# Kernel optimization log

Hardware: AMD Instinct MI355X
Metric: run time of the kernel (lower is better)

The kernel has to match this reference:

```python
import jax, jax.numpy as jnp
import numpy as np

_S2 = 2.0 ** -0.5
_S3 = 3.0 ** -0.5
_S6 = 6.0 ** -0.5
# fairchem cg_change_mat(2): (9 decomposed) -> (9 cartesian, row-major 3x3)
_CG = np.array([
    [_S3, 0, 0, 0, _S3, 0, 0, 0, _S3],
    [0, 0, 0, 0, 0, _S2, 0, -_S2, 0],
    [0, 0, -_S2, 0, 0, 0, _S2, 0, 0],
    [0, _S2, 0, -_S2, 0, 0, 0, 0, 0],
    [0, 0, _S2, 0, 0, 0, _S2, 0, 0],
    [0, 0, 0, 0, 0, _S2, 0, _S2, 0],
    [-_S6, 0, 0, 0, 2 * _S6, 0, 0, 0, -_S6],
    [0, _S2, 0, _S2, 0, 0, 0, 0, 0],
    [-_S2, 0, 0, 0, 0, 0, 0, 0, _S2],
], dtype=np.float32)  # (9, 9)

N, C, H, G = 200000, 128, 128, 2000


def setup_inputs() -> dict:
    key = jax.random.key(0)
    ks = jax.random.split(key, 8)
    node_embedding = jax.random.normal(ks[0], (N, 9, C), jnp.float32)
    W1 = jax.random.normal(ks[1], (H, C), jnp.float32) * (C ** -0.5)
    b1 = jnp.zeros((H,), jnp.float32)
    W2 = jax.random.normal(ks[2], (H, H), jnp.float32) * (H ** -0.5)
    b2 = jnp.zeros((H,), jnp.float32)
    W3 = jax.random.normal(ks[3], (1, H), jnp.float32) * (H ** -0.5)
    b3 = jnp.zeros((1,), jnp.float32)
    w_l2 = jax.random.normal(ks[4], (1, C), jnp.float32) * (C ** -0.5)
    # 100 atoms per graph, nodes sorted by graph id
    batch = jnp.repeat(jnp.arange(G, dtype=jnp.int32), N // G)
    natoms = jnp.full((G,), N // G, dtype=jnp.int32)
    return {"node_embedding": node_embedding, "W1": W1, "b1": b1, "W2": W2,
            "b2": b2, "W3": W3, "b3": b3, "w_l2": w_l2,
            "batch": batch, "natoms": natoms}


def reference(node_embedding, W1, b1, W2, b2, W3, b3, w_l2, batch, natoms):
    cg = jnp.asarray(_CG)
    n_graphs = natoms.shape[0]
    inv_natoms = 1.0 / natoms.astype(node_embedding.dtype)
    # scalar (l=0) branch: SiLU MLP on m=0 component -> per-node scalar
    x0 = node_embedding[:, 0, :]                       # (N, C)
    h = jax.nn.silu(x0 @ W1.T + b1)                    # (N, H)
    h = jax.nn.silu(h @ W2.T + b2)                     # (N, H)
    node_scalar = (h @ W3.T + b3)[:, 0]                # (N,)
    iso = jax.ops.segment_sum(node_scalar, batch, num_segments=n_graphs)
    iso = iso * inv_natoms                             # (G,) reduce='mean'
    # l=2 branch: SO3_Linear (per-l channel mix, out=1), keep m in 4:9
    node_l2 = jnp.einsum('nmc,c->nm', node_embedding[:, 4:9, :], w_l2[0])  # (N, 5)
    aniso = jax.ops.segment_sum(node_l2, batch, num_segments=n_graphs)
    aniso = aniso * inv_natoms[:, None]                # (G, 5)
    # compose_tensor: dec = [trace, 0,0,0, l2_symmetric]; r2 = dec @ CG
    dec = jnp.concatenate(
        [iso[:, None], jnp.zeros((n_graphs, 3), iso.dtype), aniso], axis=1)  # (G, 9)
    stress = (dec @ cg).reshape(-1, 3, 3)              # (G, 3, 3)
    return stress
```

## Files before the change

kernel.cpp:

```cpp
#include <hip/hip_runtime.h>

typedef __attribute__((ext_vector_type(8))) short short8;
typedef __attribute__((ext_vector_type(4))) float f32x4;
typedef unsigned int u32;
typedef unsigned short u16;

#define C_DIM 128
#define MT_MAX 7
#define XROWS 112
#define THREADS 512

__device__ __align__(16) u16 g_wpack[2][2][8][4][64][8];

__device__ __forceinline__ u16 bf16_rn(float x) {
    u32 u = __float_as_uint(x);
    u32 r = u + 0x7FFFu + ((u >> 16) & 1u);
    return (u16)(r >> 16);
}

__device__ __forceinline__ float silu_f(float x) {
    return x / (1.0f + __expf(-x));
}

__device__ __forceinline__ float dot4(float4 a, float4 b) {
    return a.x * b.x + a.y * b.y + a.z * b.z + a.w * b.w;
}

__device__ __forceinline__ void cvt4(float4 v, u32& hi01, u32& hi23, u32& lo01, u32& lo23) {
    u16 h0 = bf16_rn(v.x), h1 = bf16_rn(v.y), h2 = bf16_rn(v.z), h3 = bf16_rn(v.w);
    float r0 = v.x - __uint_as_float((u32)h0 << 16);
    float r1 = v.y - __uint_as_float((u32)h1 << 16);
    float r2 = v.z - __uint_as_float((u32)h2 << 16);
    float r3 = v.w - __uint_as_float((u32)h3 << 16);
    u16 l0 = bf16_rn(r0), l1 = bf16_rn(r1), l2 = bf16_rn(r2), l3 = bf16_rn(r3);
    hi01 = (u32)h0 | ((u32)h1 << 16);
    hi23 = (u32)h2 | ((u32)h3 << 16);
    lo01 = (u32)l0 | ((u32)l1 << 16);
    lo23 = (u32)l2 | ((u32)l3 << 16);
}

__constant__ float CG_TAB[6][9] = {
    {  0.5773502691896258f, 0.f, 0.f,  0.f, 0.5773502691896258f, 0.f,  0.f, 0.f, 0.5773502691896258f },
    {  0.f, 0.f, 0.7071067811865476f,  0.f, 0.f, 0.f,  0.7071067811865476f, 0.f, 0.f },
    {  0.f, 0.f, 0.f,  0.f, 0.f, 0.7071067811865476f,  0.f, 0.7071067811865476f, 0.f },
    { -0.4082482904638630f, 0.f, 0.f,  0.f, 0.8164965809277260f, 0.f,  0.f, 0.f, -0.4082482904638630f },
    {  0.f, 0.7071067811865476f, 0.f,  0.7071067811865476f, 0.f, 0.f,  0.f, 0.f, 0.f },
    { -0.7071067811865476f, 0.f, 0.f,  0.f, 0.f, 0.f,  0.f, 0.f, 0.7071067811865476f },
};

extern "C" __global__ void __launch_bounds__(512)
prep_wpack(const float* __restrict__ W1, const float* __restrict__ W2) {
    const int t = blockIdx.x * 512 + threadIdx.x;
    const int layer = t >> 11;
    const int rem   = t & 2047;
    const int nt    = rem >> 8;
    const int ks    = (rem >> 6) & 3;
    const int lane  = rem & 63;
    const int j  = nt * 16 + (lane & 15);
    const int k0 = ks * 32 + (lane >> 4) * 8;
    const float* W = layer ? W2 : W1;
    const float* src = W + j * C_DIM + k0;
    short8 vh, vl;
    #pragma unroll
    for (int i = 0; i < 8; ++i) {
        const float v = src[i];
        const u16 h = bf16_rn(v);
        vh[i] = (short)h;
        vl[i] = (short)bf16_rn(v - __uint_as_float((u32)h << 16));
    }
    *(short8*)&g_wpack[layer][0][nt][ks][lane][0] = vh;
    *(short8*)&g_wpack[layer][1][nt][ks][lane][0] = vl;
}

__device__ __forceinline__ void gemm_layer_pk(const u16* __restrict__ wpk_hi,
                                              const u16* __restrict__ wpk_lo,
                                              const u16* sXhi, const u16* sXlo,
                                              int w, int l, f32x4 acc[4][2]) {
    const int mt0 = (w >> 2) * 4;
    const int nt0 = (w & 3) * 2;
    const int lr  = l & 15;
    #pragma unroll
    for (int i = 0; i < 4; ++i)
        #pragma unroll
        for (int t = 0; t < 2; ++t)
            acc[i][t] = (f32x4){0.f, 0.f, 0.f, 0.f};
    #pragma unroll
    for (int ks = 0; ks < 4; ++ks) {
        const int k0 = ks * 32 + (l >> 4) * 8;
        short8 bh[2], bl[2];
        #pragma unroll
        for (int t = 0; t < 2; ++t) {
            const int idx = (((nt0 + t) * 4 + ks) * 64 + l) * 8;
            bh[t] = *(const short8*)(wpk_hi + idx);
            bl[t] = *(const short8*)(wpk_lo + idx);
        }
        #pragma unroll
        for (int i = 0; i < 4; ++i) {
            const int mt = mt0 + i;
            if (mt < MT_MAX) {
                const int row = mt * 16 + lr;
                const int off = row * 128 + (k0 ^ ((row & 7) << 3));
                short8 ah = *(const short8*)(sXhi + off);
                short8 al = *(const short8*)(sXlo + off);
                #pragma unroll
                for (int t = 0; t < 2; ++t) {
                    acc[i][t] = __builtin_amdgcn_mfma_f32_16x16x32_bf16(ah, bh[t], acc[i][t], 0, 0, 0);
                    acc[i][t] = __builtin_amdgcn_mfma_f32_16x16x32_bf16(ah, bl[t], acc[i][t], 0, 0, 0);
                    acc[i][t] = __builtin_amdgcn_mfma_f32_16x16x32_bf16(al, bh[t], acc[i][t], 0, 0, 0);
                }
            }
        }
    }
}

extern "C" __global__ void __launch_bounds__(THREADS, 4)
fused_stress(const float* __restrict__ emb,
             const float* __restrict__ b1,
             const float* __restrict__ b2,
             const float* __restrict__ W3, const float* __restrict__ b3,
             const float* __restrict__ wl2, const int* __restrict__ natoms,
             float* __restrict__ out, int NPG) {
    __shared__ u16 sXhi[XROWS * 128];
    __shared__ u16 sXlo[XROWS * 128];
    __shared__ float s_acc[6];

    const int tid = threadIdx.x;
    const int l   = tid & 63;
    const int w   = tid >> 6;
    const int lr  = l & 15;
    const int lkg = l >> 4;
    const int g   = blockIdx.x;
    const size_t nodebase = (size_t)g * (size_t)NPG;

    if (tid < 6) s_acc[tid] = 0.0f;

    #pragma unroll 4
    for (int f = tid; f < XROWS * 32; f += THREADS) {
        const int row = f >> 5, c4 = f & 31;
        float4 v = make_float4(0.f, 0.f, 0.f, 0.f);
        if (row < NPG)
            v = *((const float4*)(emb + (nodebase + row) * 9 * C_DIM) + c4);
        const int ksw = (c4 * 4) ^ ((row & 7) << 3);
        u32 a, b, c, d;
        cvt4(v, a, b, c, d);
        *(uint2*)(&sXhi[row * 128 + ksw]) = make_uint2(a, b);
        *(uint2*)(&sXlo[row * 128 + ksw]) = make_uint2(c, d);
    }

    {
        const float4 wv = *((const float4*)wl2 + (l & 31));
        float a0 = 0.f, a1 = 0.f, a2 = 0.f, a3 = 0.f, a4 = 0.f;
        for (int node = w * 2 + (l >> 5); node < NPG; node += 16) {
            const float4* p = (const float4*)(emb + (nodebase + node) * 9 * C_DIM + 4 * C_DIM) + (l & 31);
            float4 v0 = p[0];
            float4 v1 = p[32];
            float4 v2 = p[64];
            float4 v3 = p[96];
            float4 v4 = p[128];
            a0 += dot4(v0, wv);
            a1 += dot4(v1, wv);
            a2 += dot4(v2, wv);
            a3 += dot4(v3, wv);
            a4 += dot4(v4, wv);
        }
        #pragma unroll
        for (int s = 1; s < 32; s <<= 1) {
            a0 += __shfl_xor(a0, s);
            a1 += __shfl_xor(a1, s);
            a2 += __shfl_xor(a2, s);
            a3 += __shfl_xor(a3, s);
            a4 += __shfl_xor(a4, s);
        }
        if ((l & 31) == 0) {
            atomicAdd(&s_acc[1], a0);
            atomicAdd(&s_acc[2], a1);
            atomicAdd(&s_acc[3], a2);
            atomicAdd(&s_acc[4], a3);
            atomicAdd(&s_acc[5], a4);
        }
    }
    __syncthreads();

    f32x4 acc[4][2];
    const int mt0 = (w >> 2) * 4;
    const int nt0 = (w & 3) * 2;

    gemm_layer_pk(&g_wpack[0][0][0][0][0][0], &g_wpack[0][1][0][0][0][0],
                  sXhi, sXlo, w, l, acc);
    __syncthreads();

    {
        #pragma unroll
        for (int t = 0; t < 2; ++t) {
            const int j = (nt0 + t) * 16 + lr;
            const float bj = b1[j];
            #pragma unroll
            for (int i = 0; i < 4; ++i) {
                const int mt = mt0 + i;
                if (mt < MT_MAX) {
                    #pragma unroll
                    for (int r = 0; r < 4; ++r) {
                        const int row = mt * 16 + lkg * 4 + r;
                        const float hv = silu_f(acc[i][t][r] + bj);
                        const u16 hh = bf16_rn(hv);
                        const float hf = __uint_as_float((u32)hh << 16);
                        const u16 hl = bf16_rn(hv - hf);
                        const int off = row * 128 + (j ^ ((row & 7) << 3));
                        sXhi[off] = hh;
                        sXlo[off] = hl;
                    }
                }
            }
        }
    }
    __syncthreads();

    gemm_layer_pk(&g_wpack[1][0][0][0][0][0], &g_wpack[1][1][0][0][0][0],
                  sXhi, sXlo, w, l, acc);
    {
        float w3j[2], b2j[2];
        #pragma unroll
        for (int t = 0; t < 2; ++t) {
            const int j = (nt0 + t) * 16 + lr;
            w3j[t] = W3[j];
            b2j[t] = b2[j];
        }
        #pragma unroll
        for (int i = 0; i < 4; ++i) {
            const int mt = mt0 + i;
            if (mt < MT_MAX) {
                #pragma unroll
                for (int r = 0; r < 4; ++r) {
                    float p = silu_f(acc[i][0][r] + b2j[0]) * w3j[0]
                            + silu_f(acc[i][1][r] + b2j[1]) * w3j[1];
                    p += __shfl_xor(p, 1);
                    p += __shfl_xor(p, 2);
                    p += __shfl_xor(p, 4);
                    p += __shfl_xor(p, 8);
                    const int row = mt * 16 + lkg * 4 + r;
                    if (lr == 0 && row < NPG)
                        atomicAdd(&s_acc[0], p);
                }
            }
        }
    }
    __syncthreads();

    if (tid < 9) {
        const float inv = 1.0f / (float)natoms[g];
        const float iso = (s_acc[0] + (float)NPG * b3[0]) * inv;
        float o = iso * CG_TAB[0][tid];
        #pragma unroll
        for (int m = 0; m < 5; ++m)
            o += (s_acc[1 + m] * inv) * CG_TAB[1 + m][tid];
        out[(size_t)g * 9 + tid] = o;
    }
}

extern "C" void kernel_launch(void* const* d_in, const int* in_sizes, int n_in,
                              void* d_out, int out_size, void* d_ws, size_t ws_size,
                              hipStream_t stream) {
    const float* emb    = (const float*)d_in[0];
    const float* W1     = (const float*)d_in[1];
    const float* b1     = (const float*)d_in[2];
    const float* W2     = (const float*)d_in[3];
    const float* b2     = (const float*)d_in[4];
    const float* W3     = (const float*)d_in[5];
    const float* b3     = (const float*)d_in[6];
    const float* wl2    = (const float*)d_in[7];
    const int*   natoms = (const int*)d_in[9];

    const int G   = in_sizes[9];
    const int N   = in_sizes[0] / (9 * C_DIM);
    const int NPG = N / G;

    prep_wpack<<<8, 512, 0, stream>>>(W1, W2);
    fused_stress<<<G, THREADS, 0, stream>>>(emb, b1, b2, W3, b3, wl2,
                                            natoms, (float*)d_out, NPG);
}
```

Baseline: 163.9 us.

## Drop split-bf16 activations, halve block size, and prefetch packed weights

```diff
diff --git a/kernel.cpp b/kernel.cpp
--- a/kernel.cpp
+++ b/kernel.cpp
@@ -6,9 +6,10 @@
 typedef unsigned short u16;
 
 #define C_DIM 128
-#define MT_MAX 7
+#define MT 7
 #define XROWS 112
-#define THREADS 512
+#define THREADS 256
+#define WPK_PLANE 16384
 
 __device__ __align__(16) u16 g_wpack[2][2][8][4][64][8];
 
@@ -24,19 +25,6 @@
 
 __device__ __forceinline__ float dot4(float4 a, float4 b) {
     return a.x * b.x + a.y * b.y + a.z * b.z + a.w * b.w;
-}
-
-__device__ __forceinline__ void cvt4(float4 v, u32& hi01, u32& hi23, u32& lo01, u32& lo23) {
-    u16 h0 = bf16_rn(v.x), h1 = bf16_rn(v.y), h2 = bf16_rn(v.z), h3 = bf16_rn(v.w);
-    float r0 = v.x - __uint_as_float((u32)h0 << 16);
-    float r1 = v.y - __uint_as_float((u32)h1 << 16);
-    float r2 = v.z - __uint_as_float((u32)h2 << 16);
-    float r3 = v.w - __uint_as_float((u32)h3 << 16);
-    u16 l0 = bf16_rn(r0), l1 = bf16_rn(r1), l2 = bf16_rn(r2), l3 = bf16_rn(r3);
-    hi01 = (u32)h0 | ((u32)h1 << 16);
-    hi23 = (u32)h2 | ((u32)h3 << 16);
-    lo01 = (u32)l0 | ((u32)l1 << 16);
-    lo23 = (u32)l2 | ((u32)l3 << 16);
 }
 
 __constant__ float CG_TAB[6][9] = {
@@ -72,44 +60,43 @@
     *(short8*)&g_wpack[layer][1][nt][ks][lane][0] = vl;
 }
 
-__device__ __forceinline__ void gemm_layer_pk(const u16* __restrict__ wpk_hi,
-                                              const u16* __restrict__ wpk_lo,
-                                              const u16* sXhi, const u16* sXlo,
-                                              int w, int l, f32x4 acc[4][2]) {
-    const int mt0 = (w >> 2) * 4;
-    const int nt0 = (w & 3) * 2;
-    const int lr  = l & 15;
+__device__ __forceinline__ void gemm_layer_pk(const u16* __restrict__ wpk,
+                                              const u16* __restrict__ sX,
+                                              int nt0, int l, f32x4 acc[MT][2]) {
+    const int lr = l & 15;
+    const u16* base0 = wpk + (((nt0    ) * 4) * 64 + l) * 8;
+    const u16* base1 = wpk + (((nt0 + 1) * 4) * 64 + l) * 8;
     #pragma unroll
-    for (int i = 0; i < 4; ++i)
-        #pragma unroll
-        for (int t = 0; t < 2; ++t)
-            acc[i][t] = (f32x4){0.f, 0.f, 0.f, 0.f};
+    for (int mt = 0; mt < MT; ++mt) {
+        acc[mt][0] = (f32x4){0.f, 0.f, 0.f, 0.f};
+        acc[mt][1] = (f32x4){0.f, 0.f, 0.f, 0.f};
+    }
+    short8 bh0 = *(const short8*)(base0);
+    short8 bl0 = *(const short8*)(base0 + WPK_PLANE);
+    short8 bh1 = *(const short8*)(base1);
+    short8 bl1 = *(const short8*)(base1 + WPK_PLANE);
     #pragma unroll
     for (int ks = 0; ks < 4; ++ks) {
+        short8 nh0, nl0, nh1, nl1;
+        if (ks < 3) {
+            const int o = (ks + 1) * 512;
+            nh0 = *(const short8*)(base0 + o);
+            nl0 = *(const short8*)(base0 + WPK_PLANE + o);
+            nh1 = *(const short8*)(base1 + o);
+            nl1 = *(const short8*)(base1 + WPK_PLANE + o);
+        }
         const int k0 = ks * 32 + (l >> 4) * 8;
-        short8 bh[2], bl[2];
-        #pragma unroll
-        for (int t = 0; t < 2; ++t) {
-            const int idx = (((nt0 + t) * 4 + ks) * 64 + l) * 8;
-            bh[t] = *(const short8*)(wpk_hi + idx);
-            bl[t] = *(const short8*)(wpk_lo + idx);
-        }
-        #pragma unroll
-        for (int i = 0; i < 4; ++i) {
-            const int mt = mt0 + i;
-            if (mt < MT_MAX) {
-                const int row = mt * 16 + lr;
-                const int off = row * 128 + (k0 ^ ((row & 7) << 3));
-                short8 ah = *(const short8*)(sXhi + off);
-                short8 al = *(const short8*)(sXlo + off);
-                #pragma unroll
-                for (int t = 0; t < 2; ++t) {
-                    acc[i][t] = __builtin_amdgcn_mfma_f32_16x16x32_bf16(ah, bh[t], acc[i][t], 0, 0, 0);
-                    acc[i][t] = __builtin_amdgcn_mfma_f32_16x16x32_bf16(ah, bl[t], acc[i][t], 0, 0, 0);
-                    acc[i][t] = __builtin_amdgcn_mfma_f32_16x16x32_bf16(al, bh[t], acc[i][t], 0, 0, 0);
-                }
-            }
-        }
+        #pragma unroll
+        for (int mt = 0; mt < MT; ++mt) {
+            const int row = mt * 16 + lr;
+            const int off = row * 128 + (k0 ^ ((row & 7) << 3));
+            short8 ah = *(const short8*)(sX + off);
+            acc[mt][0] = __builtin_amdgcn_mfma_f32_16x16x32_bf16(ah, bh0, acc[mt][0], 0, 0, 0);
+            acc[mt][0] = __builtin_amdgcn_mfma_f32_16x16x32_bf16(ah, bl0, acc[mt][0], 0, 0, 0);
+            acc[mt][1] = __builtin_amdgcn_mfma_f32_16x16x32_bf16(ah, bh1, acc[mt][1], 0, 0, 0);
+            acc[mt][1] = __builtin_amdgcn_mfma_f32_16x16x32_bf16(ah, bl1, acc[mt][1], 0, 0, 0);
+        }
+        bh0 = nh0; bl0 = nl0; bh1 = nh1; bl1 = nl1;
     }
 }
 
@@ -120,8 +107,7 @@
              const float* __restrict__ W3, const float* __restrict__ b3,
              const float* __restrict__ wl2, const int* __restrict__ natoms,
              float* __restrict__ out, int NPG) {
-    __shared__ u16 sXhi[XROWS * 128];
-    __shared__ u16 sXlo[XROWS * 128];
+    __shared__ u16 sX[XROWS * 128];
     __shared__ float s_acc[6];
 
     const int tid = threadIdx.x;
@@ -133,6 +119,7 @@
     const size_t nodebase = (size_t)g * (size_t)NPG;
 
     if (tid < 6) s_acc[tid] = 0.0f;
+    __syncthreads();
 
     #pragma unroll 4
     for (int f = tid; f < XROWS * 32; f += THREADS) {
@@ -141,16 +128,15 @@
         if (row < NPG)
             v = *((const float4*)(emb + (nodebase + row) * 9 * C_DIM) + c4);
         const int ksw = (c4 * 4) ^ ((row & 7) << 3);
-        u32 a, b, c, d;
-        cvt4(v, a, b, c, d);
-        *(uint2*)(&sXhi[row * 128 + ksw]) = make_uint2(a, b);
-        *(uint2*)(&sXlo[row * 128 + ksw]) = make_uint2(c, d);
+        u32 p01 = (u32)bf16_rn(v.x) | ((u32)bf16_rn(v.y) << 16);
+        u32 p23 = (u32)bf16_rn(v.z) | ((u32)bf16_rn(v.w) << 16);
+        *(uint2*)(&sX[row * 128 + ksw]) = make_uint2(p01, p23);
     }
 
     {
         const float4 wv = *((const float4*)wl2 + (l & 31));
         float a0 = 0.f, a1 = 0.f, a2 = 0.f, a3 = 0.f, a4 = 0.f;
-        for (int node = w * 2 + (l >> 5); node < NPG; node += 16) {
+        for (int node = w * 2 + (l >> 5); node < NPG; node += 8) {
             const float4* p = (const float4*)(emb + (nodebase + node) * 9 * C_DIM + 4 * C_DIM) + (l & 31);
             float4 v0 = p[0];
             float4 v1 = p[32];
@@ -181,12 +167,10 @@
     }
     __syncthreads();
 
-    f32x4 acc[4][2];
-    const int mt0 = (w >> 2) * 4;
-    const int nt0 = (w & 3) * 2;
-
-    gemm_layer_pk(&g_wpack[0][0][0][0][0][0], &g_wpack[0][1][0][0][0][0],
-                  sXhi, sXlo, w, l, acc);
+    f32x4 acc[MT][2];
+    const int nt0 = w * 2;
+
+    gemm_layer_pk(&g_wpack[0][0][0][0][0][0], sX, nt0, l, acc);
     __syncthreads();
 
     {
@@ -195,28 +179,19 @@
             const int j = (nt0 + t) * 16 + lr;
             const float bj = b1[j];
             #pragma unroll
-            for (int i = 0; i < 4; ++i) {
-                const int mt = mt0 + i;
-                if (mt < MT_MAX) {
-                    #pragma unroll
-                    for (int r = 0; r < 4; ++r) {
-                        const int row = mt * 16 + lkg * 4 + r;
-                        const float hv = silu_f(acc[i][t][r] + bj);
-                        const u16 hh = bf16_rn(hv);
-                        const float hf = __uint_as_float((u32)hh << 16);
-                        const u16 hl = bf16_rn(hv - hf);
-                        const int off = row * 128 + (j ^ ((row & 7) << 3));
-                        sXhi[off] = hh;
-                        sXlo[off] = hl;
-                    }
+            for (int mt = 0; mt < MT; ++mt) {
+                #pragma unroll
+                for (int r = 0; r < 4; ++r) {
+                    const int row = mt * 16 + lkg * 4 + r;
+                    const float hv = silu_f(acc[mt][t][r] + bj);
+                    sX[row * 128 + (j ^ ((row & 7) << 3))] = bf16_rn(hv);
                 }
             }
         }
     }
     __syncthreads();
 
-    gemm_layer_pk(&g_wpack[1][0][0][0][0][0], &g_wpack[1][1][0][0][0][0],
-                  sXhi, sXlo, w, l, acc);
+    gemm_layer_pk(&g_wpack[1][0][0][0][0][0], sX, nt0, l, acc);
     {
         float w3j[2], b2j[2];
         #pragma unroll
@@ -225,24 +200,23 @@
             w3j[t] = W3[j];
             b2j[t] = b2[j];
         }
-        #pragma unroll
-        for (int i = 0; i < 4; ++i) {
-            const int mt = mt0 + i;
-            if (mt < MT_MAX) {
-                #pragma unroll
-                for (int r = 0; r < 4; ++r) {
-                    float p = silu_f(acc[i][0][r] + b2j[0]) * w3j[0]
-                            + silu_f(acc[i][1][r] + b2j[1]) * w3j[1];
-                    p += __shfl_xor(p, 1);
-                    p += __shfl_xor(p, 2);
-                    p += __shfl_xor(p, 4);
-                    p += __shfl_xor(p, 8);
-                    const int row = mt * 16 + lkg * 4 + r;
-                    if (lr == 0 && row < NPG)
-                        atomicAdd(&s_acc[0], p);
+        float psum = 0.0f;
+        #pragma unroll
+        for (int mt = 0; mt < MT; ++mt) {
+            #pragma unroll
+            for (int r = 0; r < 4; ++r) {
+                const int row = mt * 16 + lkg * 4 + r;
+                if (row < NPG) {
+                    psum += silu_f(acc[mt][0][r] + b2j[0]) * w3j[0]
+                          + silu_f(acc[mt][1][r] + b2j[1]) * w3j[1];
                 }
             }
         }
+        #pragma unroll
+        for (int s = 1; s < 64; s <<= 1)
+            psum += __shfl_xor(psum, s);
+        if (l == 0)
+            atomicAdd(&s_acc[0], psum);
     }
     __syncthreads();
 
```

Result: no change. 165.2 us (+0.8%).
